# Optimization experiments

Measured on AMD Instinct MI355X. Metric: run time of the kernel, lower is better.

The kernel has to match this reference:

```python
import jax, jax.numpy as jnp
import numpy as np

BS, N_PER, EMBED, ENC, L, OUT = 8, 8192, 128, 512, 512, 256
N = BS * N_PER          # total batched nodes
E_PER = 131072          # edges per graph (avg degree 16)
N_HE = 4096             # number of hyperedges (global over batched graph)
P = 1048576             # hyperedge incidence pairs


def _lin(k, i, o):
    return (jax.random.normal(k, (i, o), jnp.float32) / np.sqrt(i)).astype(jnp.float32)


def setup_inputs() -> dict:
    key = jax.random.key(0)
    ks = jax.random.split(key, 16)
    x = jax.random.normal(ks[0], (BS, L, ENC), jnp.float32)
    node_features = jax.random.normal(ks[1], (BS, N_PER, EMBED), jnp.float32)
    # block-diagonal batched graph (dgl.batch semantics): edges stay within each graph
    off = (jnp.arange(BS, dtype=jnp.int32) * N_PER)[:, None]
    src = (jax.random.randint(ks[2], (BS, E_PER), 0, N_PER) + off).reshape(-1)
    dst = (jax.random.randint(ks[3], (BS, E_PER), 0, N_PER) + off).reshape(-1)
    edge_index = jnp.stack([src, dst])                      # [2, E]
    hn = jax.random.randint(ks[4], (P,), 0, N)              # incident node ids
    he = jax.random.randint(ks[5], (P,), 0, N_HE)           # incident hyperedge ids
    hyperedge_index = jnp.stack([hn, he], axis=1)           # [P, 2], transposed in forward like the torch code
    return {
        "x": x, "node_features": node_features,
        "edge_index": edge_index, "hyperedge_index": hyperedge_index,
        "Wg1": _lin(ks[6], EMBED, EMBED), "bg1": jnp.zeros((EMBED,), jnp.float32),
        "Wg2": _lin(ks[7], EMBED, EMBED), "bg2": jnp.zeros((EMBED,), jnp.float32),
        "Wh1": _lin(ks[8], EMBED, EMBED), "bh1": jnp.zeros((EMBED,), jnp.float32),
        "Wh2": _lin(ks[9], EMBED, EMBED), "bh2": jnp.zeros((EMBED,), jnp.float32),
        "Wm": _lin(ks[10], ENC, EMBED), "bm": jnp.zeros((EMBED,), jnp.float32),
        "Wm2": _lin(ks[11], EMBED, EMBED), "bm2": jnp.zeros((EMBED,), jnp.float32),
        "Ws": _lin(ks[12], ENC + EMBED, OUT // 2), "bs_": jnp.zeros((OUT // 2,), jnp.float32),
        "Wt": _lin(ks[13], ENC + EMBED, OUT // 2), "bt": jnp.zeros((OUT // 2,), jnp.float32),
    }


def _gconv(h, src, dst, W, b):
    # DGL GraphConv, norm='both', allow_zero_in_degree (degrees clamped to 1)
    ones = jnp.ones(src.shape, h.dtype)
    dout = jnp.maximum(jax.ops.segment_sum(ones, src, num_segments=N), 1.0)
    din = jnp.maximum(jax.ops.segment_sum(ones, dst, num_segments=N), 1.0)
    h = h * jax.lax.rsqrt(dout)[:, None]
    h = h @ W
    agg = jax.ops.segment_sum(h[src], dst, num_segments=N)
    return agg * jax.lax.rsqrt(din)[:, None] + b


def _hconv(h, pn, pe, W, b):
    # PyG HypergraphConv with hyperedge_weight=None (ones): X' = D^-1 H B^-1 H^T (X Theta) + bias
    h = h @ W
    ones = jnp.ones(pn.shape, h.dtype)
    D = jax.ops.segment_sum(ones, pn, num_segments=N)       # node hyper-degree
    B = jax.ops.segment_sum(ones, pe, num_segments=N_HE)    # hyperedge size
    Dinv = jnp.where(D > 0, 1.0 / D, 0.0)
    Binv = jnp.where(B > 0, 1.0 / B, 0.0)
    ef = Binv[:, None] * jax.ops.segment_sum(h[pn], pe, num_segments=N_HE)
    out = Dinv[:, None] * jax.ops.segment_sum(ef[pe], pn, num_segments=N)
    return out + b


def reference(x, node_features, edge_index, hyperedge_index,
              Wg1, bg1, Wg2, bg2, Wh1, bh1, Wh2, bh2,
              Wm, bm, Wm2, bm2, Ws, bs_, Wt, bt):
    src, dst = edge_index[0], edge_index[1]
    hidx = hyperedge_index.T                 # matches torch .transpose(0, 1)
    pn, pe = hidx[0], hidx[1]
    nfr = node_features.reshape(N, EMBED)    # concatenated per-graph node features

    h = _gconv(nfr, src, dst, Wg1, bg1)
    h = _hconv(h, pn, pe, Wh1, bh1)
    h = jax.nn.relu(h) + nfr
    h = _gconv(h, src, dst, Wg2, bg2)
    h = _hconv(h, pn, pe, Wh2, bh2)
    h = jax.nn.relu(h) + nfr

    g = h.reshape(BS, N_PER, EMBED)          # equal node counts -> pad/split is a reshape
    q = jax.nn.relu(x @ Wm + bm)             # [BS, L, EMBED]
    k = jax.nn.relu(jnp.einsum('bnd,de->bne', g, Wm2) + bm2)
    C = jnp.einsum('bld,bnd->bln', q, k)     # cross-attention scores
    H = jnp.einsum('bln,bnd->bld', jax.nn.softmax(C, axis=2), g)
    cat = jnp.concatenate([x, H], axis=2)    # [BS, L, ENC+EMBED]
    G1 = jax.nn.sigmoid(cat @ Ws + bs_)
    G2 = jnp.tanh(cat @ Wt + bt)
    return jnp.concatenate([G1, G2], axis=2)  # [BS, L, OUT], dropout is identity at eval
```

## Files before the change

kernel.cpp:

```cpp
#include <hip/hip_runtime.h>
#include <hip/hip_bf16.h>

#define BSZ   8
#define NPER  8192
#define NNODE 65536
#define EPG   131072
#define EMB   128
#define ENCD  512
#define LQ    512
#define NHE   4096
#define NE    1048576
#define NP    1048576
#define NROW  4096
#define NSPLIT 16
#define SLOT_N 64
#define SLOT_E 384
#define CAP_E  10240
#define CAP_PN 10240
#define CAP_PE 18432

typedef _Float16 f16;
typedef _Float16 f16x2 __attribute__((ext_vector_type(2)));
typedef _Float16 f16x4 __attribute__((ext_vector_type(4)));
typedef _Float16 f16x8 __attribute__((ext_vector_type(8)));
typedef float f32x4 __attribute__((ext_vector_type(4)));
typedef unsigned short u16;
typedef unsigned int u32;

__global__ __launch_bounds__(256) void k_bin(const int* __restrict__ eidx,
    const int* __restrict__ hidx, int* __restrict__ du, int* __restrict__ gcur,
    u32* __restrict__ bin_e, u32* __restrict__ bin_pn, u32* __restrict__ bin_pe)
{
  __shared__ int lh[320];
  __shared__ int gb[320];
  const int tid = threadIdx.x;
  for (int i = tid; i < 320; i += 256) lh[i] = 0;
  __syncthreads();
  if (blockIdx.x < 512){
    const int eb4 = blockIdx.x*512;
    int4 sa = ((const int4*)eidx)[eb4 + tid];
    int4 sb = ((const int4*)eidx)[eb4 + 256 + tid];
    int4 da = ((const int4*)(eidx + NE))[eb4 + tid];
    int4 db = ((const int4*)(eidx + NE))[eb4 + 256 + tid];
    int ss[8] = {sa.x,sa.y,sa.z,sa.w, sb.x,sb.y,sb.z,sb.w};
    int dd[8] = {da.x,da.y,da.z,da.w, db.x,db.y,db.z,db.w};
    int rr[8];
    #pragma unroll
    for (int u = 0; u < 8; ++u){
      atomicAdd(&du[ss[u]], 1);
      rr[u] = atomicAdd(&lh[dd[u] >> 9], 1);
    }
    __syncthreads();
    if (tid < 128 && lh[tid]) gb[tid] = atomicAdd(&gcur[tid], lh[tid]);
    __syncthreads();
    #pragma unroll
    for (int u = 0; u < 8; ++u){
      int b = dd[u] >> 9;
      int pos = gb[b] + rr[u];
      if (pos < CAP_E)
        bin_e[(size_t)b*CAP_E + pos] = (u32)(dd[u] & 0xffff) | ((u32)ss[u] << 16);
    }
  } else {
    const int pb4 = (blockIdx.x - 512)*1024;
    int4 pa = ((const int4*)hidx)[pb4 + tid];
    int4 pb = ((const int4*)hidx)[pb4 + 256 + tid];
    int4 pc = ((const int4*)hidx)[pb4 + 512 + tid];
    int4 pd = ((const int4*)hidx)[pb4 + 768 + tid];
    int pn[8] = {pa.x,pa.z, pb.x,pb.z, pc.x,pc.z, pd.x,pd.z};
    int pe[8] = {pa.y,pa.w, pb.y,pb.w, pc.y,pc.w, pd.y,pd.w};
    int rn[8], re[8];
    #pragma unroll
    for (int u = 0; u < 8; ++u){
      rn[u] = atomicAdd(&lh[128 + (pn[u] >> 9)], 1);
      re[u] = atomicAdd(&lh[256 + (pe[u] >> 6)], 1);
    }
    __syncthreads();
    if (tid < 192 && lh[128 + tid]) gb[128 + tid] = atomicAdd(&gcur[128 + tid], lh[128 + tid]);
    __syncthreads();
    #pragma unroll
    for (int u = 0; u < 8; ++u){
      int bn = pn[u] >> 9;
      int pos = gb[128 + bn] + rn[u];
      if (pos < CAP_PN)
        bin_pn[(size_t)bn*CAP_PN + pos] = (u32)pn[u] | ((u32)pe[u] << 16);
      int be = pe[u] >> 6;
      int pos2 = gb[256 + be] + re[u];
      if (pos2 < CAP_PE)
        bin_pe[(size_t)be*CAP_PE + pos2] = (u32)pe[u] | ((u32)pn[u] << 16);
    }
  }
}

__global__ __launch_bounds__(256) void k_csr(const int* __restrict__ gcur,
    const u32* __restrict__ bin_e, const u32* __restrict__ bin_pn,
    const u32* __restrict__ bin_pe,
    int* __restrict__ cnt_dst, u16* __restrict__ csr_dst,
    int* __restrict__ cnt_pn, u16* __restrict__ csr_pn,
    int* __restrict__ cnt_pe, u16* __restrict__ csr_pe)
{
  const int tid = threadIdx.x;
  if (blockIdx.x < 256){
    __shared__ int cur[512];
    const int isP = blockIdx.x >= 128;
    const int b = blockIdx.x & 127;
    cur[tid] = 0; cur[tid + 256] = 0;
    __syncthreads();
    const int n0 = b*512;
    const int cap = isP ? CAP_PN : CAP_E;
    int raw = gcur[isP ? 128 + b : b];
    int count = raw < cap ? raw : cap;
    const u32* bin = (isP ? bin_pn : bin_e) + (size_t)b*cap;
    u16* csr = isP ? csr_pn : csr_dst;
    for (int i = tid; i < count; i += 256){
      u32 v = bin[i];
      int row = v & 0xffff, val = v >> 16;
      int c = atomicAdd(&cur[row - n0], 1);
      if (c < SLOT_N) csr[(size_t)row*SLOT_N + c] = (u16)val;
    }
    __syncthreads();
    int* cnt = isP ? cnt_pn : cnt_dst;
    cnt[n0 + tid]       = cur[tid];
    cnt[n0 + 256 + tid] = cur[tid + 256];
  } else {
    __shared__ int cur[64];
    const int b = blockIdx.x - 256;
    if (tid < 64) cur[tid] = 0;
    __syncthreads();
    const int e0 = b*64;
    int raw = gcur[256 + b];
    int count = raw < CAP_PE ? raw : CAP_PE;
    const u32* bin = bin_pe + (size_t)b*CAP_PE;
    for (int i = tid; i < count; i += 256){
      u32 v = bin[i];
      int row = v & 0xffff, val = v >> 16;
      int c = atomicAdd(&cur[row - e0], 1);
      if (c < SLOT_E) csr_pe[(size_t)row*SLOT_E + c] = (u16)val;
    }
    __syncthreads();
    if (tid < 64) cnt_pe[e0 + tid] = cur[tid];
  }
}

__global__ __launch_bounds__(256) void k_pre(const float* __restrict__ nfr,
    const int* __restrict__ du, f16* __restrict__ out)
{
  int i = blockIdx.x*256 + threadIdx.x;
  int node = i >> 6, j = i & 63;
  float ds = rsqrtf(fmaxf((float)du[node], 1.f));
  float2 v = ((const float2*)(nfr + (size_t)node*128))[j];
  f16x2 o = { (f16)(v.x*ds), (f16)(v.y*ds) };
  ((f16x2*)(out + (size_t)node*128))[j] = o;
}

__global__ __launch_bounds__(256) void k_gagg16(const int* __restrict__ cnt,
    const u16* __restrict__ csr, const f16* __restrict__ src, f16* __restrict__ agg)
{
  const int wv = threadIdx.x >> 6, lane = threadIdx.x & 63;
  const int blk = blockIdx.x;
  const int n = (blk & 7)*NPER + (blk >> 3)*4 + wv;
  const int nd = cnt[n];
  const int c = nd < SLOT_N ? nd : SLOT_N;
  const u16* row = csr + (size_t)n*SLOT_N;
  const f16x2* s2 = (const f16x2*)src;
  float ax = 0.f, ay = 0.f;
  if (c > 0){
    const int i0 = row[0];
    #pragma unroll 1
    for (int b = 0; b < 8; ++b){
      if (b*8 >= c) break;
      int4 iv = *(const int4*)(row + b*8);
      int ix[8] = { iv.x & 0xffff, (iv.x >> 16) & 0xffff,
                    iv.y & 0xffff, (iv.y >> 16) & 0xffff,
                    iv.z & 0xffff, (iv.z >> 16) & 0xffff,
                    iv.w & 0xffff, (iv.w >> 16) & 0xffff };
      f16x2 vv[8];
      #pragma unroll
      for (int k = 0; k < 8; ++k){
        int id = (b*8 + k < c) ? ix[k] : i0;
        vv[k] = s2[(size_t)id*64 + lane];
      }
      #pragma unroll
      for (int k = 0; k < 8; ++k){
        if (b*8 + k < c){ ax += (float)vv[k].x; ay += (float)vv[k].y; }
      }
    }
  }
  ((f16x2*)(agg + (size_t)n*128))[lane] = (f16x2){ (f16)ax, (f16)ay };
}

__global__ __launch_bounds__(256) void k_hea16(const int* __restrict__ cnt,
    const u16* __restrict__ csr, const f16* __restrict__ src, float* __restrict__ ef)
{
  const int wv = threadIdx.x >> 6, lane = threadIdx.x & 63;
  const int e = blockIdx.x*4 + wv;
  const int nd = cnt[e];
  const int n = nd < SLOT_E ? nd : SLOT_E;
  const u16* row = csr + (size_t)e*SLOT_E;
  const f16x2* s2 = (const f16x2*)src;
  float ax = 0.f, ay = 0.f;
  int j = 0;
  for (; j + 7 < n; j += 8){
    int p0 = row[j],   p1 = row[j+1], p2 = row[j+2], p3 = row[j+3];
    int p4 = row[j+4], p5 = row[j+5], p6 = row[j+6], p7 = row[j+7];
    f16x2 v0 = s2[(size_t)p0*64 + lane];
    f16x2 v1 = s2[(size_t)p1*64 + lane];
    f16x2 v2 = s2[(size_t)p2*64 + lane];
    f16x2 v3 = s2[(size_t)p3*64 + lane];
    f16x2 v4 = s2[(size_t)p4*64 + lane];
    f16x2 v5 = s2[(size_t)p5*64 + lane];
    f16x2 v6 = s2[(size_t)p6*64 + lane];
    f16x2 v7 = s2[(size_t)p7*64 + lane];
    ax += (((float)v0.x + (float)v1.x) + ((float)v2.x + (float)v3.x))
        + (((float)v4.x + (float)v5.x) + ((float)v6.x + (float)v7.x));
    ay += (((float)v0.y + (float)v1.y) + ((float)v2.y + (float)v3.y))
        + (((float)v4.y + (float)v5.y) + ((float)v6.y + (float)v7.y));
  }
  for (; j < n; ++j){
    f16x2 v = s2[(size_t)row[j]*64 + lane];
    ax += (float)v.x; ay += (float)v.y;
  }
  float s = nd > 0 ? 1.f/(float)nd : 0.f;
  ((float2*)(ef + (size_t)e*128))[lane] = make_float2(ax*s, ay*s);
}

template<int MODE, int IN16>
__global__ __launch_bounds__(256, 2) void k_gemm(const void* __restrict__ inp,
    const float* __restrict__ W, const int* __restrict__ cnt,
    const float* __restrict__ bias, void* __restrict__ outp)
{
  __shared__ float Wl[128*128];
  __shared__ float Rl[32*128];
  const int tid = threadIdx.x;
  const int rbase = blockIdx.x*32;
  for (int i = tid; i < 16384; i += 256) Wl[i] = W[i];
  if (IN16){
    const f16x2* s2 = (const f16x2*)(((const f16*)inp) + (size_t)rbase*128);
    for (int i = tid; i < 2048; i += 256){
      f16x2 v = s2[i];
      ((float2*)Rl)[i] = make_float2((float)v.x, (float)v.y);
    }
  } else {
    const float* src = ((const float*)inp) + (size_t)rbase*128;
    for (int i = tid; i < 4096; i += 256) Rl[i] = src[i];
  }
  __syncthreads();
  const int c0 = (tid & 31)*4;
  const int r0 = (tid >> 5)*4;
  f32x4 acc[4];
  #pragma unroll
  for (int j = 0; j < 4; ++j) acc[j] = (f32x4){0.f,0.f,0.f,0.f};
  for (int d = 0; d < 128; d += 4){
    f32x4 w0 = *(const f32x4*)&Wl[(d+0)*128 + c0];
    f32x4 w1 = *(const f32x4*)&Wl[(d+1)*128 + c0];
    f32x4 w2 = *(const f32x4*)&Wl[(d+2)*128 + c0];
    f32x4 w3 = *(const f32x4*)&Wl[(d+3)*128 + c0];
    #pragma unroll
    for (int j = 0; j < 4; ++j){
      f32x4 rr = *(const f32x4*)&Rl[(r0+j)*128 + d];
      acc[j] += rr.x*w0 + rr.y*w1 + rr.z*w2 + rr.w*w3;
    }
  }
  #pragma unroll
  for (int j = 0; j < 4; ++j){
    const int row = rbase + r0 + j;
    if (MODE == 0){
      *(f32x4*)(((float*)outp) + (size_t)row*128 + c0) = acc[j];
    } else if (MODE == 1){
      float sc = rsqrtf(fmaxf((float)cnt[row], 1.f));
      f16* o = ((f16*)outp) + (size_t)row*128 + c0;
      #pragma unroll
      for (int k = 0; k < 4; ++k) o[k] = (f16)(acc[j][k]*sc + bias[c0+k]);
    } else if (MODE == 2){
      f16* o = ((f16*)outp) + (size_t)row*128 + c0;
      #pragma unroll
      for (int k = 0; k < 4; ++k) o[k] = (f16)fmaxf(acc[j][k] + bias[c0+k], 0.f);
    } else {
      f16* o = ((f16*)outp) + (size_t)row*128 + c0;
      #pragma unroll
      for (int k = 0; k < 4; ++k) o[k] = (f16)acc[j][k];
    }
  }
}

template<int PRES>
__global__ __launch_bounds__(256) void k_nha(const int* __restrict__ cnt,
    const u16* __restrict__ csr, const f16* __restrict__ ef,
    const float* __restrict__ bias, const float* __restrict__ nfr,
    const int* __restrict__ du, f16* __restrict__ outp)
{
  const int wv = threadIdx.x >> 6, lane = threadIdx.x & 63;
  const int n = blockIdx.x*4 + wv;
  const int nd = cnt[n];
  const int c = nd < SLOT_N ? nd : SLOT_N;
  const u16* row = csr + (size_t)n*SLOT_N;
  const f16x2* s2 = (const f16x2*)ef;
  float2 nf = ((const float2*)(nfr + (size_t)n*128))[lane];
  float e0 = PRES ? rsqrtf(fmaxf((float)du[n], 1.f)) : 1.f;
  float ax = 0.f, ay = 0.f;
  if (c > 0){
    const int i0 = row[0];
    #pragma unroll 1
    for (int b = 0; b < 8; ++b){
      if (b*8 >= c) break;
      int4 iv = *(const int4*)(row + b*8);
      int ix[8] = { iv.x & 0xffff, (iv.x >> 16) & 0xffff,
                    iv.y & 0xffff, (iv.y >> 16) & 0xffff,
                    iv.z & 0xffff, (iv.z >> 16) & 0xffff,
                    iv.w & 0xffff, (iv.w >> 16) & 0xffff };
      f16x2 vv[8];
      #pragma unroll
      for (int k = 0; k < 8; ++k){
        int id = (b*8 + k < c) ? ix[k] : i0;
        vv[k] = s2[(size_t)id*64 + lane];
      }
      #pragma unroll
      for (int k = 0; k < 8; ++k){
        if (b*8 + k < c){ ax += (float)vv[k].x; ay += (float)vv[k].y; }
      }
    }
  }
  float bx = bias[lane*2], by = bias[lane*2+1];
  float s = nd > 0 ? 1.f/(float)nd : 0.f;
  float vx = fmaxf(ax*s + bx, 0.f) + nf.x;
  float vy = fmaxf(ay*s + by, 0.f) + nf.y;
  ((f16x2*)(outp + (size_t)n*128))[lane] = (f16x2){ (f16)(vx*e0), (f16)(vy*e0) };
}

__global__ __launch_bounds__(256) void k_gt(const f16* __restrict__ g, f16* __restrict__ gT)
{
  __shared__ f16 t[64][66];
  int b = blockIdx.z, n0 = blockIdx.x*64, c0 = blockIdx.y*64;
  for (int i = threadIdx.x; i < 64*64; i += 256){
    int n = i >> 6, c = i & 63;
    t[n][c] = g[((size_t)(b*NPER + n0 + n))*128 + c0 + c];
  }
  __syncthreads();
  for (int i = threadIdx.x; i < 64*64; i += 256){
    int c = i >> 6, n = i & 63;
    gT[((size_t)(b*128 + c0 + c))*NPER + n0 + n] = t[n][c];
  }
}

#define NCH 64
__global__ __launch_bounds__(512, 4) void k_flash(const f16* __restrict__ qb,
    const f16* __restrict__ kb, const f16* __restrict__ gT,
    f16* __restrict__ Opart, float* __restrict__ mZ)
{
  __shared__ f16 Kl[64*128];
  __shared__ f16 Vl[128*64];
  __shared__ f16 Pl[8*16*64];
  const int sp = blockIdx.x, l0 = blockIdx.y*128, b = blockIdx.z;
  const int tid = threadIdx.x;
  const int w = tid >> 6, lane = tid & 63;
  const int quad = lane >> 4, col = lane & 15;
  const int koff = quad*8;
  const int krow = tid >> 4;
  const int kc8  = tid & 15;
  const int vrow = tid >> 3;
  const int vc8  = tid & 7;

  const f16* qrow = qb + ((size_t)(b*LQ + l0 + w*16 + col))*128 + koff;
  f16x8 aq[4];
  #pragma unroll
  for (int ks = 0; ks < 4; ++ks) aq[ks] = *(const f16x8*)(qrow + ks*32);
  float mrun[4] = {-1e30f,-1e30f,-1e30f,-1e30f};
  float zrun[4] = {0.f,0.f,0.f,0.f};
  f32x4 O[8];
  #pragma unroll
  for (int i = 0; i < 8; ++i) O[i] = (f32x4){0.f,0.f,0.f,0.f};

  const int nbase = sp*(NPER/NSPLIT);
  f16x8 kr[2], vr[2];
#define LOADKV(N0)                                                           \
  { _Pragma("unroll")                                                        \
    for (int i2 = 0; i2 < 2; ++i2){                                          \
      kr[i2] = *(const f16x8*)(kb + ((size_t)(b*NPER + (N0) + krow + i2*32))*128 + kc8*8); \
      vr[i2] = *(const f16x8*)(gT + ((size_t)(b*128 + vrow + i2*64))*NPER + (N0) + vc8*8); \
    } }
  LOADKV(nbase);
  #pragma unroll 1
  for (int it = 0; it < (NPER/NSPLIT)/NCH; ++it){
    const int n0 = nbase + it*NCH;
    __syncthreads();
    #pragma unroll
    for (int i2 = 0; i2 < 2; ++i2){
      int r = krow + i2*32;
      *(f16x8*)&Kl[r*128 + ((kc8 ^ (r & 7))*8)] = kr[i2];
      int d = vrow + i2*64;
      *(f16x8*)&Vl[d*64  + ((vc8 ^ (d & 7))*8)] = vr[i2];
    }
    __syncthreads();
    if (it < (NPER/NSPLIT)/NCH - 1) LOADKV(n0 + NCH);

    f32x4 st[4];
    #pragma unroll
    for (int t = 0; t < 4; ++t){
      st[t] = (f32x4){0.f,0.f,0.f,0.f};
      const int r = t*16 + col, rs = r & 7;
      #pragma unroll
      for (int ks = 0; ks < 4; ++ks){
        f16x8 bf = *(const f16x8*)&Kl[r*128 + (((ks*4 + quad) ^ rs)*8)];
        st[t] = __builtin_amdgcn_mfma_f32_16x16x32_f16(aq[ks], bf, st[t], 0, 0, 0);
      }
    }
    float alr[4];
    #pragma unroll
    for (int r = 0; r < 4; ++r){
      float rm = st[0][r];
      #pragma unroll
      for (int t = 1; t < 4; ++t) rm = fmaxf(rm, st[t][r]);
      rm = fmaxf(rm, __shfl_xor(rm, 1));
      rm = fmaxf(rm, __shfl_xor(rm, 2));
      rm = fmaxf(rm, __shfl_xor(rm, 4));
      rm = fmaxf(rm, __shfl_xor(rm, 8));
      float mn = fmaxf(mrun[r], rm);
      float al = __expf(mrun[r] - mn);
      float ps[4], rsum = 0.f;
      #pragma unroll
      for (int t = 0; t < 4; ++t){ ps[t] = __expf(st[t][r] - mn); rsum += ps[t]; }
      rsum += __shfl_xor(rsum, 1);
      rsum += __shfl_xor(rsum, 2);
      rsum += __shfl_xor(rsum, 4);
      rsum += __shfl_xor(rsum, 8);
      zrun[r] = zrun[r]*al + rsum;
      mrun[r] = mn;
      alr[r] = al;
      const int prow = quad*4 + r, pswz = prow & 7;
      #pragma unroll
      for (int t = 0; t < 4; ++t)
        Pl[w*1024 + prow*64 + (((t*2 + (col >> 3)) ^ pswz)*8) + (col & 7)] = (f16)ps[t];
    }
    #pragma unroll
    for (int dt = 0; dt < 8; ++dt)
      #pragma unroll
      for (int r = 0; r < 4; ++r) O[dt][r] *= alr[r];
    __builtin_amdgcn_wave_barrier();
    #pragma unroll
    for (int kk = 0; kk < 2; ++kk){
      f16x8 ap = *(const f16x8*)&Pl[w*1024 + col*64 + (((kk*4 + quad) ^ (col & 7))*8)];
      #pragma unroll
      for (int dt = 0; dt < 8; ++dt){
        const int d = col + dt*16;
        f16x8 bv = *(const f16x8*)&Vl[d*64 + (((kk*4 + quad) ^ (d & 7))*8)];
        O[dt] = __builtin_amdgcn_mfma_f32_16x16x32_f16(ap, bv, O[dt], 0, 0, 0);
      }
    }
    __builtin_amdgcn_wave_barrier();
  }
#undef LOADKV
  const int growb = b*LQ + l0 + w*16 + quad*4;
  #pragma unroll
  for (int r = 0; r < 4; ++r){
    f16* od = Opart + ((size_t)sp*NROW + growb + r)*128 + col;
    #pragma unroll
    for (int dt = 0; dt < 8; ++dt) od[dt*16] = (f16)O[dt][r];
  }
  if (col == 0){
    #pragma unroll
    for (int r = 0; r < 4; ++r){
      ((float2*)mZ)[(size_t)sp*NROW + growb + r] = make_float2(mrun[r], zrun[r]);
    }
  }
}

__global__ __launch_bounds__(256) void k_comb(const f16* __restrict__ Opart,
    const float* __restrict__ mZ, f16* __restrict__ cat)
{
  int i = blockIdx.x*256 + threadIdx.x;
  int row = i >> 6, d2 = (i & 63)*2;
  float ms[NSPLIT], zs[NSPLIT];
  float M = -1e30f;
  #pragma unroll
  for (int s = 0; s < NSPLIT; ++s){
    float2 v = ((const float2*)mZ)[(size_t)s*NROW + row];
    ms[s] = v.x; zs[s] = v.y;
    M = fmaxf(M, v.x);
  }
  float Zt = 0.f, ax = 0.f, ay = 0.f;
  #pragma unroll
  for (int s = 0; s < NSPLIT; ++s){
    float e = __expf(ms[s] - M);
    Zt += zs[s]*e;
    f16x2 op = *(const f16x2*)(Opart + ((size_t)s*NROW + row)*128 + d2);
    ax += e*(float)op.x; ay += e*(float)op.y;
  }
  float inv = 1.f/Zt;
  f16x2 o = { (f16)(ax*inv), (f16)(ay*inv) };
  *(f16x2*)(cat + (size_t)row*640 + 512 + d2) = o;
}

__global__ __launch_bounds__(256) void k_prep(const float* __restrict__ x,
    const float* __restrict__ Wsg, const float* __restrict__ Wtn,
    const float* __restrict__ Wm,
    f16* __restrict__ cat, f16* __restrict__ w16, f16* __restrict__ wm16)
{
  if (blockIdx.x < 2048){
    int id = blockIdx.x*256 + threadIdx.x;
    int row = id >> 7, c4 = (id & 127)*4;
    float4 v = *(const float4*)(x + (size_t)row*512 + c4);
    f16x4 o = { (f16)v.x, (f16)v.y, (f16)v.z, (f16)v.w };
    *(f16x4*)(cat + (size_t)row*640 + c4) = o;
  } else if (blockIdx.x < 2208){
    int id = (blockIdx.x - 2048)*256 + threadIdx.x;
    int n = id / 160;
    int k0 = (id - n*160)*4;
    const float* src = n < 128 ? (Wsg + n) : (Wtn + (n - 128));
    f16x4 o = { (f16)src[(k0+0)*128], (f16)src[(k0+1)*128],
                (f16)src[(k0+2)*128], (f16)src[(k0+3)*128] };
    *(f16x4*)(w16 + (size_t)n*640 + k0) = o;
  } else {
    int id = (blockIdx.x - 2208)*256 + threadIdx.x;
    int n = id >> 7;
    int k0 = (id & 127)*4;
    const float* src = Wm + n;
    f16x4 o = { (f16)src[(k0+0)*128], (f16)src[(k0+1)*128],
                (f16)src[(k0+2)*128], (f16)src[(k0+3)*128] };
    *(f16x4*)(wm16 + (size_t)n*512 + k0) = o;
  }
}

__global__ __launch_bounds__(64) void k_qgemm2(const f16* __restrict__ cat,
    const f16* __restrict__ wm16, const float* __restrict__ bm, f16* __restrict__ q)
{
  const int lane = threadIdx.x;
  const int quad = lane >> 4, col = lane & 15;
  const int koff = quad*8;
  const int row0 = blockIdx.x * 16;
  const f16* ar = cat + (size_t)(row0 + col)*640 + koff;
  const f16* br = wm16 + (size_t)col*512 + koff;
  f32x4 acc[8];
  #pragma unroll
  for (int nt = 0; nt < 8; ++nt) acc[nt] = (f32x4){0.f,0.f,0.f,0.f};
  for (int ks = 0; ks < 16; ++ks){
    f16x8 a = *(const f16x8*)(ar + ks*32);
    #pragma unroll
    for (int nt = 0; nt < 8; ++nt){
      f16x8 b = *(const f16x8*)(br + (size_t)nt*16*512 + ks*32);
      acc[nt] = __builtin_amdgcn_mfma_f32_16x16x32_f16(a, b, acc[nt], 0, 0, 0);
    }
  }
  #pragma unroll
  for (int nt = 0; nt < 8; ++nt){
    int n = nt*16 + col;
    float bv = bm[n];
    #pragma unroll
    for (int r = 0; r < 4; ++r){
      float v = fmaxf(acc[nt][r] + bv, 0.f);
      q[(size_t)(row0 + quad*4 + r)*128 + n] = (f16)v;
    }
  }
}

__global__ __launch_bounds__(64) void k_fin2(const f16* __restrict__ cat,
    const f16* __restrict__ w16, const float* __restrict__ bsg,
    const float* __restrict__ btn, float* __restrict__ out)
{
  const int lane = threadIdx.x;
  const int quad = lane >> 4, col = lane & 15;
  const int koff = quad*8;
  const int row0 = blockIdx.x * 16;
  const f16* ar = cat + (size_t)(row0 + col)*640 + koff;
  const f16* br = w16 + (size_t)col*640 + koff;
  f32x4 acc[16];
  #pragma unroll
  for (int nt = 0; nt < 16; ++nt) acc[nt] = (f32x4){0.f,0.f,0.f,0.f};
  for (int ks = 0; ks < 20; ++ks){
    f16x8 a = *(const f16x8*)(ar + ks*32);
    #pragma unroll
    for (int nt = 0; nt < 16; ++nt){
      f16x8 b = *(const f16x8*)(br + (size_t)nt*16*640 + ks*32);
      acc[nt] = __builtin_amdgcn_mfma_f32_16x16x32_f16(a, b, acc[nt], 0, 0, 0);
    }
  }
  #pragma unroll
  for (int nt = 0; nt < 16; ++nt){
    int n = nt*16 + col;
    float bv = n < 128 ? bsg[n] : btn[n - 128];
    #pragma unroll
    for (int r = 0; r < 4; ++r){
      float v = acc[nt][r] + bv;
      v = n < 128 ? 1.f/(1.f + __expf(-v)) : tanhf(v);
      out[(size_t)(row0 + quad*4 + r)*256 + n] = v;
    }
  }
}

extern "C" void kernel_launch(void* const* d_in, const int* in_sizes, int n_in,
                              void* d_out, int out_size, void* d_ws, size_t ws_size,
                              hipStream_t stream)
{
  const float* x    = (const float*)d_in[0];
  const float* nfr  = (const float*)d_in[1];
  const int*   eidx = (const int*)d_in[2];
  const int*   hidx = (const int*)d_in[3];
  const float *Wg1=(const float*)d_in[4],  *bg1=(const float*)d_in[5];
  const float *Wg2=(const float*)d_in[6],  *bg2=(const float*)d_in[7];
  const float *Wh1=(const float*)d_in[8],  *bh1=(const float*)d_in[9];
  const float *Wh2=(const float*)d_in[10], *bh2=(const float*)d_in[11];
  const float *Wm =(const float*)d_in[12], *bm =(const float*)d_in[13];
  const float *Wm2=(const float*)d_in[14], *bm2=(const float*)d_in[15];
  const float *Wsg=(const float*)d_in[16], *bsg=(const float*)d_in[17];
  const float *Wtn=(const float*)d_in[18], *btn=(const float*)d_in[19];
  float* out = (float*)d_out;

  char* base = (char*)d_ws;
  f16*   h4_16  = (f16*)(base);
  f16*   agg16  = (f16*)(base + 33554432);
  u32*   bin_e  = (u32*)(base + 33554432);
  u32*   bin_pn = (u32*)(base + 38797312);
  u32*   bin_pe = (u32*)(base + 44040192);
  int*   gcur   = (int*)(base + 48758784);
  f16*   cat16  = (f16*)(base + 33554432);
  f16*   w16    = (f16*)(base + 38797312);
  f16*   wm16   = (f16*)(base + 39124992);
  f16*   bufA   = (f16*)(base + 67108864);
  f16*   bufB   = (f16*)(base + 83886080);
  f16*   Opart  = (f16*)(base + 67108864);
  u16*   csr_dst= (u16*)(base + 100663296);
  f16*   kb     = (f16*)(base + 100663296);
  u16*   csr_pn = (u16*)(base + 117440512);
  f16*   gT     = (f16*)(base + 117440512);
  u16*   csr_pe = (u16*)(base + 134217728);
  int*   cnt_dst= (int*)(base + 140509184);
  int*   cnt_pn = (int*)(base + 140771328);
  int*   cnt_pe = (int*)(base + 141033472);
  int*   du     = (int*)(base + 141049856);
  float* ef0    = (float*)(base + 141312000);
  f16*   ef1    = (f16*)(base + 143409152);
  f16*   qb     = (f16*)(base + 145506304);
  float* mZ     = (float*)(base + 146554880);
  const size_t needB = (size_t)147079168;
  if (ws_size < needB) return;

  hipMemsetAsync(du, 0, 262144, stream);
  hipMemsetAsync(gcur, 0, 1280, stream);
  k_bin<<<1024, 256, 0, stream>>>(eidx, hidx, du, gcur, bin_e, bin_pn, bin_pe);
  k_csr<<<320, 256, 0, stream>>>(gcur, bin_e, bin_pn, bin_pe,
                                 cnt_dst, csr_dst, cnt_pn, csr_pn, cnt_pe, csr_pe);

  k_pre<<<NNODE*64/256, 256, 0, stream>>>(nfr, du, bufA);
  k_gagg16<<<NNODE/4, 256, 0, stream>>>(cnt_dst, csr_dst, bufA, agg16);
  k_gemm<1,1><<<NNODE/32, 256, 0, stream>>>(agg16, Wg1, cnt_dst, bg1, bufB);
  k_hea16<<<NHE/4, 256, 0, stream>>>(cnt_pe, csr_pe, bufB, ef0);
  k_gemm<3,0><<<NHE/32, 256, 0, stream>>>(ef0, Wh1, nullptr, nullptr, ef1);
  k_nha<1><<<NNODE/4, 256, 0, stream>>>(cnt_pn, csr_pn, ef1, bh1, nfr, du, bufA);

  k_gagg16<<<NNODE/4, 256, 0, stream>>>(cnt_dst, csr_dst, bufA, agg16);
  k_gemm<1,1><<<NNODE/32, 256, 0, stream>>>(agg16, Wg2, cnt_dst, bg2, bufB);
  k_hea16<<<NHE/4, 256, 0, stream>>>(cnt_pe, csr_pe, bufB, ef0);
  k_gemm<3,0><<<NHE/32, 256, 0, stream>>>(ef0, Wh2, nullptr, nullptr, ef1);
  k_nha<0><<<NNODE/4, 256, 0, stream>>>(cnt_pn, csr_pn, ef1, bh2, nfr, nullptr, h4_16);

  k_prep<<<2272, 256, 0, stream>>>(x, Wsg, Wtn, Wm, cat16, w16, wm16);
  k_qgemm2<<<NROW/16, 64, 0, stream>>>(cat16, wm16, bm, qb);
  k_gemm<2,1><<<NNODE/32, 256, 0, stream>>>(h4_16, Wm2, nullptr, bm2, kb);
  k_gt<<<dim3(NPER/64, 2, BSZ), 256, 0, stream>>>(h4_16, gT);
  k_flash<<<dim3(NSPLIT, LQ/128, BSZ), 512, 0, stream>>>(qb, kb, gT, Opart, mZ);
  k_comb<<<NROW*64/256, 256, 0, stream>>>(Opart, mZ, cat16);
  k_fin2<<<NROW/16, 64, 0, stream>>>(cat16, w16, bsg, btn, out);

  (void)in_sizes; (void)n_in; (void)out_size;
}
```

Before: 647.1 us.

## Compute out-degrees via binned shared-memory histograms instead of global atomics

Out-degree counting no longer issues one global atomic per edge. Source ids are now binned per 512-node range in k_bin, and extra k_csr blocks histogram each bin in shared memory to write du directly, which also removes the du memset. k_bin blocks now each process twice as many elements, halving the grid. The cost is an extra 4 MB bin buffer write and read, plus more shared-memory atomics per block.

```diff
diff --git a/kernel.cpp b/kernel.cpp
--- a/kernel.cpp
+++ b/kernel.cpp
@@ -28,49 +28,61 @@
 typedef unsigned int u32;
 
 __global__ __launch_bounds__(256) void k_bin(const int* __restrict__ eidx,
-    const int* __restrict__ hidx, int* __restrict__ du, int* __restrict__ gcur,
-    u32* __restrict__ bin_e, u32* __restrict__ bin_pn, u32* __restrict__ bin_pe)
-{
-  __shared__ int lh[320];
-  __shared__ int gb[320];
+    const int* __restrict__ hidx, int* __restrict__ gcur,
+    u32* __restrict__ bin_e, u32* __restrict__ bin_s,
+    u32* __restrict__ bin_pn, u32* __restrict__ bin_pe)
+{
+  __shared__ int lh[448];
+  __shared__ int gb[448];
   const int tid = threadIdx.x;
-  for (int i = tid; i < 320; i += 256) lh[i] = 0;
+  for (int i = tid; i < 448; i += 256) lh[i] = 0;
   __syncthreads();
-  if (blockIdx.x < 512){
-    const int eb4 = blockIdx.x*512;
-    int4 sa = ((const int4*)eidx)[eb4 + tid];
-    int4 sb = ((const int4*)eidx)[eb4 + 256 + tid];
-    int4 da = ((const int4*)(eidx + NE))[eb4 + tid];
-    int4 db = ((const int4*)(eidx + NE))[eb4 + 256 + tid];
-    int ss[8] = {sa.x,sa.y,sa.z,sa.w, sb.x,sb.y,sb.z,sb.w};
-    int dd[8] = {da.x,da.y,da.z,da.w, db.x,db.y,db.z,db.w};
-    int rr[8];
-    #pragma unroll
-    for (int u = 0; u < 8; ++u){
-      atomicAdd(&du[ss[u]], 1);
-      rr[u] = atomicAdd(&lh[dd[u] >> 9], 1);
-    }
-    __syncthreads();
-    if (tid < 128 && lh[tid]) gb[tid] = atomicAdd(&gcur[tid], lh[tid]);
-    __syncthreads();
-    #pragma unroll
-    for (int u = 0; u < 8; ++u){
+  if (blockIdx.x < 256){
+    const int eb4 = blockIdx.x*1024;
+    int ss[16], dd[16];
+    #pragma unroll
+    for (int t = 0; t < 4; ++t){
+      int4 s4 = ((const int4*)eidx)[eb4 + t*256 + tid];
+      int4 d4 = ((const int4*)(eidx + NE))[eb4 + t*256 + tid];
+      ss[t*4+0]=s4.x; ss[t*4+1]=s4.y; ss[t*4+2]=s4.z; ss[t*4+3]=s4.w;
+      dd[t*4+0]=d4.x; dd[t*4+1]=d4.y; dd[t*4+2]=d4.z; dd[t*4+3]=d4.w;
+    }
+    int rd[16], rs[16];
+    #pragma unroll
+    for (int u = 0; u < 16; ++u){
+      rd[u] = atomicAdd(&lh[dd[u] >> 9], 1);
+      rs[u] = atomicAdd(&lh[128 + (ss[u] >> 9)], 1);
+    }
+    __syncthreads();
+    if (tid < 128){
+      if (lh[tid]) gb[tid] = atomicAdd(&gcur[tid], lh[tid]);
+    } else {
+      if (lh[tid]) gb[tid] = atomicAdd(&gcur[192 + tid], lh[tid]);
+    }
+    __syncthreads();
+    #pragma unroll
+    for (int u = 0; u < 16; ++u){
       int b = dd[u] >> 9;
-      int pos = gb[b] + rr[u];
+      int pos = gb[b] + rd[u];
       if (pos < CAP_E)
         bin_e[(size_t)b*CAP_E + pos] = (u32)(dd[u] & 0xffff) | ((u32)ss[u] << 16);
+      int bs = ss[u] >> 9;
+      int pos2 = gb[128 + bs] + rs[u];
+      if (pos2 < CAP_E)
+        bin_s[(size_t)bs*CAP_E + pos2] = (u32)(ss[u] & 0xffff);
     }
   } else {
-    const int pb4 = (blockIdx.x - 512)*1024;
-    int4 pa = ((const int4*)hidx)[pb4 + tid];
-    int4 pb = ((const int4*)hidx)[pb4 + 256 + tid];
-    int4 pc = ((const int4*)hidx)[pb4 + 512 + tid];
-    int4 pd = ((const int4*)hidx)[pb4 + 768 + tid];
-    int pn[8] = {pa.x,pa.z, pb.x,pb.z, pc.x,pc.z, pd.x,pd.z};
-    int pe[8] = {pa.y,pa.w, pb.y,pb.w, pc.y,pc.w, pd.y,pd.w};
-    int rn[8], re[8];
-    #pragma unroll
-    for (int u = 0; u < 8; ++u){
+    const int pb4 = (blockIdx.x - 256)*2048;
+    int pn[16], pe[16];
+    #pragma unroll
+    for (int t = 0; t < 8; ++t){
+      int4 p = ((const int4*)hidx)[pb4 + t*256 + tid];
+      pn[t*2+0] = p.x; pe[t*2+0] = p.y;
+      pn[t*2+1] = p.z; pe[t*2+1] = p.w;
+    }
+    int rn[16], re[16];
+    #pragma unroll
+    for (int u = 0; u < 16; ++u){
       rn[u] = atomicAdd(&lh[128 + (pn[u] >> 9)], 1);
       re[u] = atomicAdd(&lh[256 + (pe[u] >> 6)], 1);
     }
@@ -78,7 +90,7 @@
     if (tid < 192 && lh[128 + tid]) gb[128 + tid] = atomicAdd(&gcur[128 + tid], lh[128 + tid]);
     __syncthreads();
     #pragma unroll
-    for (int u = 0; u < 8; ++u){
+    for (int u = 0; u < 16; ++u){
       int bn = pn[u] >> 9;
       int pos = gb[128 + bn] + rn[u];
       if (pos < CAP_PN)
@@ -92,11 +104,12 @@
 }
 
 __global__ __launch_bounds__(256) void k_csr(const int* __restrict__ gcur,
-    const u32* __restrict__ bin_e, const u32* __restrict__ bin_pn,
-    const u32* __restrict__ bin_pe,
+    const u32* __restrict__ bin_e, const u32* __restrict__ bin_s,
+    const u32* __restrict__ bin_pn, const u32* __restrict__ bin_pe,
     int* __restrict__ cnt_dst, u16* __restrict__ csr_dst,
     int* __restrict__ cnt_pn, u16* __restrict__ csr_pn,
-    int* __restrict__ cnt_pe, u16* __restrict__ csr_pe)
+    int* __restrict__ cnt_pe, u16* __restrict__ csr_pe,
+    int* __restrict__ du)
 {
   const int tid = threadIdx.x;
   if (blockIdx.x < 256){
@@ -121,7 +134,7 @@
     int* cnt = isP ? cnt_pn : cnt_dst;
     cnt[n0 + tid]       = cur[tid];
     cnt[n0 + 256 + tid] = cur[tid + 256];
-  } else {
+  } else if (blockIdx.x < 320){
     __shared__ int cur[64];
     const int b = blockIdx.x - 256;
     if (tid < 64) cur[tid] = 0;
@@ -138,6 +151,22 @@
     }
     __syncthreads();
     if (tid < 64) cnt_pe[e0 + tid] = cur[tid];
+  } else {
+    __shared__ int cur[512];
+    const int b = blockIdx.x - 320;
+    cur[tid] = 0; cur[tid + 256] = 0;
+    __syncthreads();
+    const int n0 = b*512;
+    int raw = gcur[320 + b];
+    int count = raw < CAP_E ? raw : CAP_E;
+    const u32* bin = bin_s + (size_t)b*CAP_E;
+    for (int i = tid; i < count; i += 256){
+      int row = (int)(bin[i] & 0xffff);
+      atomicAdd(&cur[row - n0], 1);
+    }
+    __syncthreads();
+    du[n0 + tid]       = cur[tid];
+    du[n0 + 256 + tid] = cur[tid + 256];
   }
 }
 
@@ -610,6 +639,7 @@
   u32*   bin_pn = (u32*)(base + 38797312);
   u32*   bin_pe = (u32*)(base + 44040192);
   int*   gcur   = (int*)(base + 48758784);
+  u32*   bin_s  = (u32*)(base + 50331648);
   f16*   cat16  = (f16*)(base + 33554432);
   f16*   w16    = (f16*)(base + 38797312);
   f16*   wm16   = (f16*)(base + 39124992);
@@ -632,11 +662,10 @@
   const size_t needB = (size_t)147079168;
   if (ws_size < needB) return;
 
-  hipMemsetAsync(du, 0, 262144, stream);
-  hipMemsetAsync(gcur, 0, 1280, stream);
-  k_bin<<<1024, 256, 0, stream>>>(eidx, hidx, du, gcur, bin_e, bin_pn, bin_pe);
-  k_csr<<<320, 256, 0, stream>>>(gcur, bin_e, bin_pn, bin_pe,
-                                 cnt_dst, csr_dst, cnt_pn, csr_pn, cnt_pe, csr_pe);
+  hipMemsetAsync(gcur, 0, 1792, stream);
+  k_bin<<<512, 256, 0, stream>>>(eidx, hidx, gcur, bin_e, bin_s, bin_pn, bin_pe);
+  k_csr<<<448, 256, 0, stream>>>(gcur, bin_e, bin_s, bin_pn, bin_pe,
+                                 cnt_dst, csr_dst, cnt_pn, csr_pn, cnt_pe, csr_pe, du);
 
   k_pre<<<NNODE*64/256, 256, 0, stream>>>(nfr, du, bufA);
   k_gagg16<<<NNODE/4, 256, 0, stream>>>(cnt_dst, csr_dst, bufA, agg16);
```

Result: faster. 609.7 us (-5.8%).
